# Performance work log

Measured on AMD Instinct MI355X. Metric: run time of the kernel, lower is better.

The kernel has to match this reference:

```python
import jax, jax.numpy as jnp
import numpy as np

B, N, C, E, H = 2, 20000, 64, 640000, 16

def setup_inputs() -> dict:
    key = jax.random.key(0)
    ks = jax.random.split(key, 9)
    Q = jax.random.normal(ks[0], (B, N, C), dtype=jnp.float32)
    K = jax.random.normal(ks[1], (B, N, C), dtype=jnp.float32)
    V = jax.random.normal(ks[2], (B, N, C), dtype=jnp.float32)
    src = jax.random.randint(ks[3], (E,), 0, N, dtype=jnp.int32)
    dst = jax.random.randint(ks[4], (E,), 0, N, dtype=jnp.int32)
    efeat = jax.random.uniform(ks[5], (E, 2), dtype=jnp.float32)  # [s_norm, d_norm] in [0,1]
    W1 = jax.random.normal(ks[6], (2, H), dtype=jnp.float32) * 0.5
    b1 = jnp.zeros((H,), dtype=jnp.float32)
    W2 = jax.random.normal(ks[7], (H, 1), dtype=jnp.float32) * 0.5
    b2 = jnp.zeros((1,), dtype=jnp.float32)
    return {"Q": Q, "K": K, "V": V, "efeat": efeat, "W1": W1, "b1": b1,
            "W2": W2, "b2": b2, "src": src, "dst": dst}

def reference(Q, K, V, efeat, W1, b1, W2, b2, src, dst):
    n = Q.shape[1]
    # per-edge bias: MLP(e_ij) -> (E,)
    bias = (jax.nn.relu(efeat @ W1 + b1) @ W2 + b2)[:, 0]
    # per-edge logits: Q_dst . K_src  -> (E, B)
    logits = jnp.einsum('bec,bec->eb', Q[:, dst, :], K[:, src, :]) + bias[:, None]
    # segment softmax over incoming edges of each dst node
    seg_max = jax.ops.segment_max(logits, dst, num_segments=n)          # (N, B)
    exp_l = jnp.exp(logits - seg_max[dst])                               # (E, B)
    denom = jax.ops.segment_sum(exp_l, dst, num_segments=n)[dst]         # (E, B)
    alpha = exp_l / denom                                                # (E, B)
    # weighted aggregation of parent values: (E,B,C) scattered to (N,B,C)
    msg = alpha[:, :, None] * jnp.transpose(V[:, src, :], (1, 0, 2))
    H_msg = jax.ops.segment_sum(msg, dst, num_segments=n)                # (N, B, C)
    return jnp.transpose(H_msg, (1, 0, 2))                               # (B, N, C)
```

## Files before the change

kernel.cpp:

```cpp
#include <hip/hip_runtime.h>
#include <hip/hip_fp16.h>
#include <math.h>


#define EB_B 2
#define EB_C 64
#define EB_H 16

__device__ __forceinline__ unsigned f2h2(float a, float b) {
    __half2 h = __floats2half2_rn(a, b);
    return *reinterpret_cast<unsigned*>(&h);
}
__device__ __forceinline__ float2 h2f2(unsigned u) {
    __half2 h = *reinterpret_cast<__half2*>(&u);
    return __half22float2(h);
}

__global__ __launch_bounds__(256) void eb_pack_kernel(
    const float4* __restrict__ K4, const float4* __restrict__ V4,
    uint4* __restrict__ kv, int total, int* __restrict__ cnt, int N) {
    int i = blockIdx.x * blockDim.x + threadIdx.x;
    if (i < N) cnt[i] = 0;
    if (i >= total) return;
    float4 k = K4[i];
    float4 v = V4[i];
    uint4 o;
    o.x = f2h2(k.x, k.y);
    o.y = f2h2(k.z, k.w);
    o.z = f2h2(v.x, v.y);
    o.w = f2h2(v.z, v.w);
    kv[i] = o;
}

__global__ void eb_count_kernel(const int* __restrict__ dst,
                                int* __restrict__ cnt,
                                int* __restrict__ slot, int E) {
    int e = blockIdx.x * blockDim.x + threadIdx.x;
    if (e < E) slot[e] = atomicAdd(&cnt[dst[e]], 1);
}

__global__ __launch_bounds__(1024) void eb_scan1(const int* __restrict__ cnt,
                                                 int* __restrict__ offsets,
                                                 int* __restrict__ bsum, int N) {
    __shared__ int wsum[16];
    int tid = threadIdx.x;
    int wv = tid >> 6, ln = tid & 63;
    int i = blockIdx.x * 1024 + tid;
    int v = (i < N) ? cnt[i] : 0;
    int x = v;
#pragma unroll
    for (int off = 1; off < 64; off <<= 1) {
        int t = __shfl_up(x, off, 64);
        if (ln >= off) x += t;
    }
    if (ln == 63) wsum[wv] = x;
    __syncthreads();
    if (wv == 0 && ln < 16) {
        int y = wsum[ln];
#pragma unroll
        for (int off = 1; off < 16; off <<= 1) {
            int t = __shfl_up(y, off, 64);
            if (ln >= off) y += t;
        }
        wsum[ln] = y;
    }
    __syncthreads();
    int base = (wv > 0 ? wsum[wv - 1] : 0);
    if (i < N) offsets[i] = base + x - v;
    if (tid == 1023) bsum[blockIdx.x] = base + x;
}

__global__ __launch_bounds__(1024) void eb_scan3(int* __restrict__ offsets,
                                                 const int* __restrict__ bsum,
                                                 int N, int E) {
    __shared__ int s_base;
    if (threadIdx.x == 0) {
        int b = 0;
        for (int j = 0; j < (int)blockIdx.x; ++j) b += bsum[j];
        s_base = b;
    }
    __syncthreads();
    int i = blockIdx.x * 1024 + threadIdx.x;
    if (i < N) offsets[i] += s_base;
    else if (i == N) offsets[N] = E;
}

__global__ void eb_fill_kernel(const int* __restrict__ dst,
                               const int* __restrict__ src,
                               const int* __restrict__ slot,
                               const int* __restrict__ offsets,
                               const float* __restrict__ efeat,
                               const float* __restrict__ W1,
                               const float* __restrict__ b1,
                               const float* __restrict__ W2,
                               const float* __restrict__ b2,
                               int2* __restrict__ ep, int E) {
    int e = blockIdx.x * blockDim.x + threadIdx.x;
    if (e >= E) return;
    float ef0 = efeat[2 * e];
    float ef1 = efeat[2 * e + 1];
    float acc = b2[0];
#pragma unroll
    for (int h = 0; h < EB_H; ++h) {
        float a = fmaf(ef0, W1[h], fmaf(ef1, W1[EB_H + h], b1[h]));
        a = fmaxf(a, 0.0f);
        acc = fmaf(a, W2[h], acc);
    }
    int pos = offsets[dst[e]] + slot[e];
    ep[pos] = make_int2(src[e], __float_as_int(acc));
}

__global__ __launch_bounds__(256) void eb_attn_fp16_kernel(
    const float4* __restrict__ Q4, const uint4* __restrict__ kv,
    const int2* __restrict__ ep, const int* __restrict__ offsets,
    float4* __restrict__ out4, int N) {
    int wave = threadIdx.x >> 6;
    int lane = threadIdx.x & 63;
    int task = blockIdx.x * 4 + wave;
    if (task >= N * EB_B) return;
    int b = (task >= N) ? 1 : 0;
    int n = task - (b ? N : 0);
    int g = lane >> 4;
    int cl = lane & 15;
    const size_t brow = (size_t)N * 16;
    float4 q = Q4[(size_t)b * brow + (size_t)n * 16 + cl];
    const uint4* kvb = kv + (size_t)b * brow;
    int start = offsets[n];
    int end = offsets[n + 1];
    int nit = (end - start + 7) >> 3;

    float m = -1e30f, s = 0.0f;
    float ax = 0.0f, ay = 0.0f, az = 0.0f, aw = 0.0f;

    for (int it = 0; it < nit; ++it) {
        int e0 = start + it * 8 + g;
        int e1 = e0 + 4;
        bool v0 = e0 < end;
        bool v1 = e1 < end;
        int2 md0 = ep[v0 ? e0 : 0];
        int2 md1 = ep[v1 ? e1 : 0];
        uint4 u0 = kvb[(size_t)md0.x * 16 + cl];
        uint4 u1 = kvb[(size_t)md1.x * 16 + cl];
        float2 k0a = h2f2(u0.x), k0b = h2f2(u0.y);
        float2 k1a = h2f2(u1.x), k1b = h2f2(u1.y);
        float p0 = fmaf(q.x, k0a.x, fmaf(q.y, k0a.y,
                   fmaf(q.z, k0b.x, q.w * k0b.y)));
        float p1 = fmaf(q.x, k1a.x, fmaf(q.y, k1a.y,
                   fmaf(q.z, k1b.x, q.w * k1b.y)));
        p0 += __shfl_xor(p0, 1);  p1 += __shfl_xor(p1, 1);
        p0 += __shfl_xor(p0, 2);  p1 += __shfl_xor(p1, 2);
        p0 += __shfl_xor(p0, 4);  p1 += __shfl_xor(p1, 4);
        p0 += __shfl_xor(p0, 8);  p1 += __shfl_xor(p1, 8);
        float l0 = v0 ? p0 + __int_as_float(md0.y) : -INFINITY;
        float l1 = v1 ? p1 + __int_as_float(md1.y) : -INFINITY;
        float mn = fmaxf(m, fmaxf(l0, l1));
        float sc = __expf(m - mn);
        float w0 = __expf(l0 - mn);
        float w1 = __expf(l1 - mn);
        float2 va0 = h2f2(u0.z), vb0 = h2f2(u0.w);
        float2 va1 = h2f2(u1.z), vb1 = h2f2(u1.w);
        s  = fmaf(s, sc, w0 + w1);
        ax = fmaf(ax, sc, fmaf(w0, va0.x, w1 * va1.x));
        ay = fmaf(ay, sc, fmaf(w0, va0.y, w1 * va1.y));
        az = fmaf(az, sc, fmaf(w0, vb0.x, w1 * vb1.x));
        aw = fmaf(aw, sc, fmaf(w0, vb0.y, w1 * vb1.y));
        m = mn;
    }

    float m1 = fmaxf(m, __shfl_xor(m, 16));
    float mA = fmaxf(m1, __shfl_xor(m1, 32));
    float scale = __expf(m - mA);
    s *= scale; ax *= scale; ay *= scale; az *= scale; aw *= scale;
    s  += __shfl_xor(s, 16);  s  += __shfl_xor(s, 32);
    ax += __shfl_xor(ax, 16); ax += __shfl_xor(ax, 32);
    ay += __shfl_xor(ay, 16); ay += __shfl_xor(ay, 32);
    az += __shfl_xor(az, 16); az += __shfl_xor(az, 32);
    aw += __shfl_xor(aw, 16); aw += __shfl_xor(aw, 32);

    if (lane < 16) {
        float inv = (end > start) ? 1.0f / s : 0.0f;
        float4 o;
        o.x = ax * inv; o.y = ay * inv; o.z = az * inv; o.w = aw * inv;
        out4[(size_t)b * brow + (size_t)n * 16 + cl] = o;
    }
}

__global__ __launch_bounds__(256) void eb_attn_f32_kernel(
    const float4* __restrict__ Q4, const float4* __restrict__ K4,
    const float4* __restrict__ V4,
    const int2* __restrict__ ep, const int* __restrict__ offsets,
    float4* __restrict__ out4, int N) {
    int wave = threadIdx.x >> 6;
    int lane = threadIdx.x & 63;
    int task = blockIdx.x * 4 + wave;
    if (task >= N * EB_B) return;
    int b = (task >= N) ? 1 : 0;
    int n = task - (b ? N : 0);
    int g = lane >> 4;
    int cl = lane & 15;
    const size_t brow = (size_t)N * 16;
    const float4* Qb = Q4 + (size_t)b * brow;
    const float4* Kb = K4 + (size_t)b * brow;
    const float4* Vb = V4 + (size_t)b * brow;
    float4 q = Qb[(size_t)n * 16 + cl];
    int start = offsets[n];
    int end = offsets[n + 1];
    int nit = (end - start + 3) >> 2;

    float m = -1e30f, s = 0.0f;
    float ax = 0.0f, ay = 0.0f, az = 0.0f, aw = 0.0f;
    for (int it = 0; it < nit; ++it) {
        int ei = start + it * 4 + g;
        bool valid = ei < end;
        int2 md = ep[valid ? ei : 0];
        int sv = md.x;
        float4 k = Kb[(size_t)sv * 16 + cl];
        float4 v = Vb[(size_t)sv * 16 + cl];
        float p = fmaf(q.x, k.x, fmaf(q.y, k.y, fmaf(q.z, k.z, q.w * k.w)));
        p += __shfl_xor(p, 1);
        p += __shfl_xor(p, 2);
        p += __shfl_xor(p, 4);
        p += __shfl_xor(p, 8);
        float l = valid ? p + __int_as_float(md.y) : -INFINITY;
        float mn = fmaxf(m, l);
        float sc = __expf(m - mn);
        float w  = __expf(l - mn);
        s  = fmaf(s, sc, w);
        ax = fmaf(ax, sc, w * v.x);
        ay = fmaf(ay, sc, w * v.y);
        az = fmaf(az, sc, w * v.z);
        aw = fmaf(aw, sc, w * v.w);
        m = mn;
    }
    float m1 = fmaxf(m, __shfl_xor(m, 16));
    float mA = fmaxf(m1, __shfl_xor(m1, 32));
    float scale = __expf(m - mA);
    s *= scale; ax *= scale; ay *= scale; az *= scale; aw *= scale;
    s  += __shfl_xor(s, 16);  s  += __shfl_xor(s, 32);
    ax += __shfl_xor(ax, 16); ax += __shfl_xor(ax, 32);
    ay += __shfl_xor(ay, 16); ay += __shfl_xor(ay, 32);
    az += __shfl_xor(az, 16); az += __shfl_xor(az, 32);
    aw += __shfl_xor(aw, 16); aw += __shfl_xor(aw, 32);
    if (lane < 16) {
        float inv = (end > start) ? 1.0f / s : 0.0f;
        float4 o;
        o.x = ax * inv; o.y = ay * inv; o.z = az * inv; o.w = aw * inv;
        out4[(size_t)b * brow + (size_t)n * 16 + cl] = o;
    }
}

extern "C" void kernel_launch(void* const* d_in, const int* in_sizes, int n_in,
                              void* d_out, int out_size, void* d_ws, size_t ws_size,
                              hipStream_t stream) {
    const float* Q     = (const float*)d_in[0];
    const float* K     = (const float*)d_in[1];
    const float* V     = (const float*)d_in[2];
    const float* efeat = (const float*)d_in[3];
    const float* W1    = (const float*)d_in[4];
    const float* b1    = (const float*)d_in[5];
    const float* W2    = (const float*)d_in[6];
    const float* b2    = (const float*)d_in[7];
    const int*   src   = (const int*)d_in[8];
    const int*   dst   = (const int*)d_in[9];
    float* out = (float*)d_out;

    const int E = in_sizes[8];
    const int N = in_sizes[0] / (EB_B * EB_C);

    char* base = (char*)d_ws;
    size_t off = 0;
    auto take = [&](size_t nbytes) {
        char* p = base + off;
        off += (nbytes + 15) & ~(size_t)15;
        return p;
    };
    int* offsets = (int*)take((size_t)(N + 1) * 4);
    int* cnt     = (int*)take((size_t)N * 4);
    int* bsum    = (int*)take(64 * 4);
    int* slot    = (int*)take((size_t)E * 4);
    int2* ep     = (int2*)take((size_t)E * 8);
    uint4* kv    = (uint4*)take((size_t)EB_B * N * 16 * sizeof(uint4));
    bool use_fp16 = off <= ws_size;

    int tpb = 256;
    int NB = (N + 1023) >> 10;
    if (use_fp16) {
        int total = EB_B * N * 16;
        eb_pack_kernel<<<(total + tpb - 1) / tpb, tpb, 0, stream>>>(
            (const float4*)K, (const float4*)V, kv, total, cnt, N);
    } else {
        eb_pack_kernel<<<(N + tpb - 1) / tpb, tpb, 0, stream>>>(
            (const float4*)K, (const float4*)V, kv, 0, cnt, N);
    }
    eb_count_kernel<<<(E + tpb - 1) / tpb, tpb, 0, stream>>>(dst, cnt, slot, E);
    eb_scan1<<<NB, 1024, 0, stream>>>(cnt, offsets, bsum, N);
    eb_scan3<<<(N + 1024) >> 10, 1024, 0, stream>>>(offsets, bsum, N, E);
    eb_fill_kernel<<<(E + tpb - 1) / tpb, tpb, 0, stream>>>(
        dst, src, slot, offsets, efeat, W1, b1, W2, b2, ep, E);

    int tasks = N * EB_B;
    if (use_fp16) {
        eb_attn_fp16_kernel<<<(tasks + 3) / 4, tpb, 0, stream>>>(
            (const float4*)Q, kv, ep, offsets, (float4*)out, N);
    } else {
        eb_attn_f32_kernel<<<(tasks + 3) / 4, tpb, 0, stream>>>(
            (const float4*)Q, (const float4*)K, (const float4*)V,
            ep, offsets, (float4*)out, N);
    }
}
```

Measured before the change: 99.09 us.

## Prefetch edge data in attention, use fdot2, single-pass decoupled scan, vectorized count

The fp16 attention loop now software-pipelines its gathers. It loads the KV rows for the next iteration and the edge metadata two iterations ahead, so gather latency overlaps with compute. The dot product uses packed fp16 fdot2 with Q converted to half. The two-kernel scan becomes one kernel with a decoupled look-back on flags, and the count kernel processes four edges per thread with int4 loads. Converting Q to fp16 loses precision, and the look-back spin relies on earlier blocks being scheduled first.

Measured after the change: 104.2 us. 5.2% more time.

```diff
diff --git a/kernel.cpp b/kernel.cpp
--- a/kernel.cpp
+++ b/kernel.cpp
@@ -7,6 +7,8 @@
 #define EB_C 64
 #define EB_H 16
 
+typedef _Float16 h2v __attribute__((ext_vector_type(2)));
+
 __device__ __forceinline__ unsigned f2h2(float a, float b) {
     __half2 h = __floats2half2_rn(a, b);
     return *reinterpret_cast<unsigned*>(&h);
@@ -15,43 +17,63 @@
     __half2 h = *reinterpret_cast<__half2*>(&u);
     return __half22float2(h);
 }
-
-__global__ __launch_bounds__(256) void eb_pack_kernel(
+__device__ __forceinline__ h2v bch2(unsigned u) {
+    h2v r;
+    __builtin_memcpy(&r, &u, 4);
+    return r;
+}
+
+__global__ __launch_bounds__(256) void eb_pack(
     const float4* __restrict__ K4, const float4* __restrict__ V4,
-    uint4* __restrict__ kv, int total, int* __restrict__ cnt, int N) {
+    uint4* __restrict__ kv, int total,
+    int* __restrict__ cnt, int* __restrict__ flags, int N) {
     int i = blockIdx.x * blockDim.x + threadIdx.x;
     if (i < N) cnt[i] = 0;
+    if (i < 32) flags[i] = 0;
     if (i >= total) return;
     float4 k = K4[i];
     float4 v = V4[i];
     uint4 o;
-    o.x = f2h2(k.x, k.y);
-    o.y = f2h2(k.z, k.w);
-    o.z = f2h2(v.x, v.y);
-    o.w = f2h2(v.z, v.w);
+    o.x = f2h2(k.x, k.y); o.y = f2h2(k.z, k.w);
+    o.z = f2h2(v.x, v.y); o.w = f2h2(v.z, v.w);
     kv[i] = o;
 }
 
-__global__ void eb_count_kernel(const int* __restrict__ dst,
-                                int* __restrict__ cnt,
-                                int* __restrict__ slot, int E) {
-    int e = blockIdx.x * blockDim.x + threadIdx.x;
+__global__ void eb_count4(const int4* __restrict__ dst4,
+                          int* __restrict__ cnt,
+                          int4* __restrict__ slot4, int E4) {
+    int i = blockIdx.x * blockDim.x + threadIdx.x;
+    if (i >= E4) return;
+    int4 d = dst4[i];
+    int4 s;
+    s.x = atomicAdd(&cnt[d.x], 1);
+    s.y = atomicAdd(&cnt[d.y], 1);
+    s.z = atomicAdd(&cnt[d.z], 1);
+    s.w = atomicAdd(&cnt[d.w], 1);
+    slot4[i] = s;
+}
+__global__ void eb_count1(const int* __restrict__ dst,
+                          int* __restrict__ cnt,
+                          int* __restrict__ slot, int lo, int E) {
+    int e = lo + blockIdx.x * blockDim.x + threadIdx.x;
     if (e < E) slot[e] = atomicAdd(&cnt[dst[e]], 1);
 }
 
-__global__ __launch_bounds__(1024) void eb_scan1(const int* __restrict__ cnt,
-                                                 int* __restrict__ offsets,
-                                                 int* __restrict__ bsum, int N) {
+__global__ __launch_bounds__(1024) void eb_scan(const int* __restrict__ cnt,
+                                                int* __restrict__ offsets,
+                                                int* __restrict__ flags,
+                                                int N, int E) {
     __shared__ int wsum[16];
-    int tid = threadIdx.x;
-    int wv = tid >> 6, ln = tid & 63;
-    int i = blockIdx.x * 1024 + tid;
+    __shared__ int s_agg, s_base;
+    const int b = blockIdx.x, t = threadIdx.x;
+    const int ln = t & 63, wv = t >> 6;
+    const int i = (b << 10) + t;
     int v = (i < N) ? cnt[i] : 0;
     int x = v;
 #pragma unroll
     for (int off = 1; off < 64; off <<= 1) {
-        int t = __shfl_up(x, off, 64);
-        if (ln >= off) x += t;
+        int tv = __shfl_up(x, off, 64);
+        if (ln >= off) x += tv;
     }
     if (ln == 63) wsum[wv] = x;
     __syncthreads();
@@ -59,29 +81,26 @@
         int y = wsum[ln];
 #pragma unroll
         for (int off = 1; off < 16; off <<= 1) {
-            int t = __shfl_up(y, off, 64);
-            if (ln >= off) y += t;
+            int tv = __shfl_up(y, off, 64);
+            if (ln >= off) y += tv;
         }
         wsum[ln] = y;
     }
     __syncthreads();
-    int base = (wv > 0 ? wsum[wv - 1] : 0);
-    if (i < N) offsets[i] = base + x - v;
-    if (tid == 1023) bsum[blockIdx.x] = base + x;
-}
-
-__global__ __launch_bounds__(1024) void eb_scan3(int* __restrict__ offsets,
-                                                 const int* __restrict__ bsum,
-                                                 int N, int E) {
-    __shared__ int s_base;
-    if (threadIdx.x == 0) {
-        int b = 0;
-        for (int j = 0; j < (int)blockIdx.x; ++j) b += bsum[j];
-        s_base = b;
-    }
+    if (t == 1023) s_agg = wsum[15];
     __syncthreads();
-    int i = blockIdx.x * 1024 + threadIdx.x;
-    if (i < N) offsets[i] += s_base;
+    if (t == 0) {
+        int base = 0;
+        if (b > 0) {
+            while ((base = atomicAdd(&flags[b - 1], 0)) == 0) {}
+            base -= 1;
+        }
+        atomicExch(&flags[b], base + s_agg + 1);
+        s_base = base;
+    }
+    __syncthreads();
+    int local_excl = (wv > 0 ? wsum[wv - 1] : 0) + x - v;
+    if (i < N) offsets[i] = s_base + local_excl;
     else if (i == N) offsets[N] = E;
 }
 
@@ -89,7 +108,7 @@
                                const int* __restrict__ src,
                                const int* __restrict__ slot,
                                const int* __restrict__ offsets,
-                               const float* __restrict__ efeat,
+                               const float2* __restrict__ efeat2,
                                const float* __restrict__ W1,
                                const float* __restrict__ b1,
                                const float* __restrict__ W2,
@@ -97,12 +116,11 @@
                                int2* __restrict__ ep, int E) {
     int e = blockIdx.x * blockDim.x + threadIdx.x;
     if (e >= E) return;
-    float ef0 = efeat[2 * e];
-    float ef1 = efeat[2 * e + 1];
+    float2 ef = efeat2[e];
     float acc = b2[0];
 #pragma unroll
     for (int h = 0; h < EB_H; ++h) {
-        float a = fmaf(ef0, W1[h], fmaf(ef1, W1[EB_H + h], b1[h]));
+        float a = fmaf(ef.x, W1[h], fmaf(ef.y, W1[EB_H + h], b1[h]));
         a = fmaxf(a, 0.0f);
         acc = fmaf(a, W2[h], acc);
     }
@@ -110,7 +128,7 @@
     ep[pos] = make_int2(src[e], __float_as_int(acc));
 }
 
-__global__ __launch_bounds__(256) void eb_attn_fp16_kernel(
+__global__ __launch_bounds__(256) void eb_attn_fp16(
     const float4* __restrict__ Q4, const uint4* __restrict__ kv,
     const int2* __restrict__ ep, const int* __restrict__ offsets,
     float4* __restrict__ out4, int N) {
@@ -123,36 +141,46 @@
     int g = lane >> 4;
     int cl = lane & 15;
     const size_t brow = (size_t)N * 16;
-    float4 q = Q4[(size_t)b * brow + (size_t)n * 16 + cl];
+    float4 qf = Q4[(size_t)b * brow + (size_t)n * 16 + cl];
+    h2v q01; q01[0] = (_Float16)qf.x; q01[1] = (_Float16)qf.y;
+    h2v q23; q23[0] = (_Float16)qf.z; q23[1] = (_Float16)qf.w;
     const uint4* kvb = kv + (size_t)b * brow;
     int start = offsets[n];
     int end = offsets[n + 1];
     int nit = (end - start + 7) >> 3;
 
+    int eP = start + g;
+    int2 c0 = ep[eP < end ? eP : 0];
+    int2 c1 = ep[eP + 4 < end ? eP + 4 : 0];
+    uint4 u0 = kvb[(size_t)c0.x * 16 + cl];
+    uint4 u1 = kvb[(size_t)c1.x * 16 + cl];
+    int eN = start + 8 + g;
+    int2 n0 = ep[eN < end ? eN : 0];
+    int2 n1 = ep[eN + 4 < end ? eN + 4 : 0];
+
     float m = -1e30f, s = 0.0f;
     float ax = 0.0f, ay = 0.0f, az = 0.0f, aw = 0.0f;
 
     for (int it = 0; it < nit; ++it) {
+        uint4 fu0 = kvb[(size_t)n0.x * 16 + cl];
+        uint4 fu1 = kvb[(size_t)n1.x * 16 + cl];
+        int e2 = start + (it + 2) * 8 + g;
+        int2 nn0 = ep[e2 < end ? e2 : 0];
+        int2 nn1 = ep[e2 + 4 < end ? e2 + 4 : 0];
         int e0 = start + it * 8 + g;
         int e1 = e0 + 4;
         bool v0 = e0 < end;
         bool v1 = e1 < end;
-        int2 md0 = ep[v0 ? e0 : 0];
-        int2 md1 = ep[v1 ? e1 : 0];
-        uint4 u0 = kvb[(size_t)md0.x * 16 + cl];
-        uint4 u1 = kvb[(size_t)md1.x * 16 + cl];
-        float2 k0a = h2f2(u0.x), k0b = h2f2(u0.y);
-        float2 k1a = h2f2(u1.x), k1b = h2f2(u1.y);
-        float p0 = fmaf(q.x, k0a.x, fmaf(q.y, k0a.y,
-                   fmaf(q.z, k0b.x, q.w * k0b.y)));
-        float p1 = fmaf(q.x, k1a.x, fmaf(q.y, k1a.y,
-                   fmaf(q.z, k1b.x, q.w * k1b.y)));
+        float p0 = __builtin_amdgcn_fdot2(q01, bch2(u0.x),
+                   __builtin_amdgcn_fdot2(q23, bch2(u0.y), 0.0f, false), false);
+        float p1 = __builtin_amdgcn_fdot2(q01, bch2(u1.x),
+                   __builtin_amdgcn_fdot2(q23, bch2(u1.y), 0.0f, false), false);
         p0 += __shfl_xor(p0, 1);  p1 += __shfl_xor(p1, 1);
         p0 += __shfl_xor(p0, 2);  p1 += __shfl_xor(p1, 2);
         p0 += __shfl_xor(p0, 4);  p1 += __shfl_xor(p1, 4);
         p0 += __shfl_xor(p0, 8);  p1 += __shfl_xor(p1, 8);
-        float l0 = v0 ? p0 + __int_as_float(md0.y) : -INFINITY;
-        float l1 = v1 ? p1 + __int_as_float(md1.y) : -INFINITY;
+        float l0 = v0 ? p0 + __int_as_float(c0.y) : -INFINITY;
+        float l1 = v1 ? p1 + __int_as_float(c1.y) : -INFINITY;
         float mn = fmaxf(m, fmaxf(l0, l1));
         float sc = __expf(m - mn);
         float w0 = __expf(l0 - mn);
@@ -165,6 +193,7 @@
         az = fmaf(az, sc, fmaf(w0, vb0.x, w1 * vb1.x));
         aw = fmaf(aw, sc, fmaf(w0, vb0.y, w1 * vb1.y));
         m = mn;
+        c0 = n0; c1 = n1; u0 = fu0; u1 = fu1; n0 = nn0; n1 = nn1;
     }
 
     float m1 = fmaxf(m, __shfl_xor(m, 16));
@@ -185,7 +214,7 @@
     }
 }
 
-__global__ __launch_bounds__(256) void eb_attn_f32_kernel(
+__global__ __launch_bounds__(256) void eb_attn_f32(
     const float4* __restrict__ Q4, const float4* __restrict__ K4,
     const float4* __restrict__ V4,
     const int2* __restrict__ ep, const int* __restrict__ offsets,
@@ -199,23 +228,20 @@
     int g = lane >> 4;
     int cl = lane & 15;
     const size_t brow = (size_t)N * 16;
-    const float4* Qb = Q4 + (size_t)b * brow;
+    float4 q = Q4[(size_t)b * brow + (size_t)n * 16 + cl];
     const float4* Kb = K4 + (size_t)b * brow;
     const float4* Vb = V4 + (size_t)b * brow;
-    float4 q = Qb[(size_t)n * 16 + cl];
     int start = offsets[n];
     int end = offsets[n + 1];
     int nit = (end - start + 3) >> 2;
-
     float m = -1e30f, s = 0.0f;
     float ax = 0.0f, ay = 0.0f, az = 0.0f, aw = 0.0f;
     for (int it = 0; it < nit; ++it) {
         int ei = start + it * 4 + g;
         bool valid = ei < end;
         int2 md = ep[valid ? ei : 0];
-        int sv = md.x;
-        float4 k = Kb[(size_t)sv * 16 + cl];
-        float4 v = Vb[(size_t)sv * 16 + cl];
+        float4 k = Kb[(size_t)md.x * 16 + cl];
+        float4 v = Vb[(size_t)md.x * 16 + cl];
         float p = fmaf(q.x, k.x, fmaf(q.y, k.y, fmaf(q.z, k.z, q.w * k.w)));
         p += __shfl_xor(p, 1);
         p += __shfl_xor(p, 2);
@@ -252,20 +278,21 @@
 extern "C" void kernel_launch(void* const* d_in, const int* in_sizes, int n_in,
                               void* d_out, int out_size, void* d_ws, size_t ws_size,
                               hipStream_t stream) {
-    const float* Q     = (const float*)d_in[0];
-    const float* K     = (const float*)d_in[1];
-    const float* V     = (const float*)d_in[2];
-    const float* efeat = (const float*)d_in[3];
-    const float* W1    = (const float*)d_in[4];
-    const float* b1    = (const float*)d_in[5];
-    const float* W2    = (const float*)d_in[6];
-    const float* b2    = (const float*)d_in[7];
-    const int*   src   = (const int*)d_in[8];
-    const int*   dst   = (const int*)d_in[9];
-    float* out = (float*)d_out;
+    const float4* Q4  = (const float4*)d_in[0];
+    const float4* K4  = (const float4*)d_in[1];
+    const float4* V4  = (const float4*)d_in[2];
+    const float2* ef2 = (const float2*)d_in[3];
+    const float* W1   = (const float*)d_in[4];
+    const float* b1   = (const float*)d_in[5];
+    const float* W2   = (const float*)d_in[6];
+    const float* b2   = (const float*)d_in[7];
+    const int*   src  = (const int*)d_in[8];
+    const int*   dst  = (const int*)d_in[9];
+    float4* out4 = (float4*)d_out;
 
     const int E = in_sizes[8];
     const int N = in_sizes[0] / (EB_B * EB_C);
+    const int total = EB_B * N * 16;
 
     char* base = (char*)d_ws;
     size_t off = 0;
@@ -276,35 +303,31 @@
     };
     int* offsets = (int*)take((size_t)(N + 1) * 4);
     int* cnt     = (int*)take((size_t)N * 4);
-    int* bsum    = (int*)take(64 * 4);
+    int* flags   = (int*)take(32 * 4);
     int* slot    = (int*)take((size_t)E * 4);
     int2* ep     = (int2*)take((size_t)E * 8);
-    uint4* kv    = (uint4*)take((size_t)EB_B * N * 16 * sizeof(uint4));
+    uint4* kv    = (uint4*)take((size_t)total * 16);
     bool use_fp16 = off <= ws_size;
 
-    int tpb = 256;
-    int NB = (N + 1023) >> 10;
+    const int tpb = 256;
+    const int NB = (N + 1023) >> 10;
+    eb_pack<<<(total + tpb - 1) / tpb, tpb, 0, stream>>>(
+        K4, V4, kv, use_fp16 ? total : 0, cnt, flags, N);
+    int E4 = E >> 2;
+    if (E4 > 0)
+        eb_count4<<<(E4 + tpb - 1) / tpb, tpb, 0, stream>>>(
+            (const int4*)dst, cnt, (int4*)slot, E4);
+    if (E & 3)
+        eb_count1<<<1, 64, 0, stream>>>(dst, cnt, slot, E4 << 2, E);
+    eb_scan<<<NB, 1024, 0, stream>>>(cnt, offsets, flags, N, E);
+    eb_fill_kernel<<<(E + tpb - 1) / tpb, tpb, 0, stream>>>(
+        dst, src, slot, offsets, ef2, W1, b1, W2, b2, ep, E);
+
+    int tasks = N * EB_B;
+    int blks = (tasks + 3) / 4;
     if (use_fp16) {
-        int total = EB_B * N * 16;
-        eb_pack_kernel<<<(total + tpb - 1) / tpb, tpb, 0, stream>>>(
-            (const float4*)K, (const float4*)V, kv, total, cnt, N);
+        eb_attn_fp16<<<blks, tpb, 0, stream>>>(Q4, kv, ep, offsets, out4, N);
     } else {
-        eb_pack_kernel<<<(N + tpb - 1) / tpb, tpb, 0, stream>>>(
-            (const float4*)K, (const float4*)V, kv, 0, cnt, N);
-    }
-    eb_count_kernel<<<(E + tpb - 1) / tpb, tpb, 0, stream>>>(dst, cnt, slot, E);
-    eb_scan1<<<NB, 1024, 0, stream>>>(cnt, offsets, bsum, N);
-    eb_scan3<<<(N + 1024) >> 10, 1024, 0, stream>>>(offsets, bsum, N, E);
-    eb_fill_kernel<<<(E + tpb - 1) / tpb, tpb, 0, stream>>>(
-        dst, src, slot, offsets, efeat, W1, b1, W2, b2, ep, E);
-
-    int tasks = N * EB_B;
-    if (use_fp16) {
-        eb_attn_fp16_kernel<<<(tasks + 3) / 4, tpb, 0, stream>>>(
-            (const float4*)Q, kv, ep, offsets, (float4*)out, N);
-    } else {
-        eb_attn_f32_kernel<<<(tasks + 3) / 4, tpb, 0, stream>>>(
-            (const float4*)Q, (const float4*)K, (const float4*)V,
-            ep, offsets, (float4*)out, N);
-    }
-}
+        eb_attn_f32<<<blks, tpb, 0, stream>>>(Q4, K4, V4, ep, offsets, out4, N);
+    }
+}
```
